# Kernel tuning notes

Measured on AMD Instinct MI355X. Metric: run time of the kernel, lower is better.

Reference implementation:

```python
import jax, jax.numpy as jnp
import numpy as np

N_NODES = 100000
N_EDGES = 1600000
D = 64            # embedding_dim
D2 = D * D        # GRUCell hidden/input size


def gru_cell(x, h, w_ih, w_hh, b_ih, b_hh):
    # PyTorch GRUCell math. x, h: [D2]; w_ih, w_hh: [3*D2, D2]; b_*: [3*D2]
    gi = w_ih @ x + b_ih
    gh = w_hh @ h + b_hh
    i_r, i_z, i_n = jnp.split(gi, 3)
    h_r, h_z, h_n = jnp.split(gh, 3)
    r = jax.nn.sigmoid(i_r + h_r)
    z = jax.nn.sigmoid(i_z + h_z)
    n = jnp.tanh(i_n + r * h_n)
    return (1.0 - z) * n + z * h


def gcn_layer(x, w, src, dst, edge_norm):
    # dense transform then degree-normalized gather-scatter aggregation
    h = x @ w                                   # [N, D]
    m = h[src] * edge_norm[:, None]             # [E, D] messages
    return jax.ops.segment_sum(m, dst, num_segments=N_NODES)


def setup_inputs() -> dict:
    key = jax.random.key(0)
    ks = jax.random.split(key, 12)
    s = 0.02  # keep GRU gates in a sane range
    return {
        "node_embeddings": jax.random.normal(ks[0], (N_NODES, D), jnp.float32),
        "gc1_weights": jax.random.normal(ks[1], (D, D), jnp.float32) * s,
        "gc2_weights": jax.random.normal(ks[2], (D, D), jnp.float32) * s,
        "gc1_hist": jax.random.normal(ks[3], (D, D), jnp.float32) * s,
        "gc2_hist": jax.random.normal(ks[4], (D, D), jnp.float32) * s,
        "w_ih": jax.random.normal(ks[5], (3 * D2, D2), jnp.float32) * s,
        "w_hh": jax.random.normal(ks[6], (3 * D2, D2), jnp.float32) * s,
        "b_ih": jax.random.normal(ks[7], (3 * D2,), jnp.float32) * s,
        "b_hh": jax.random.normal(ks[8], (3 * D2,), jnp.float32) * s,
        "src": jax.random.randint(ks[9], (N_EDGES,), 0, N_NODES, jnp.int32),
        "dst": jax.random.randint(ks[10], (N_EDGES,), 0, N_NODES, jnp.int32),
    }


def reference(node_embeddings, gc1_weights, gc2_weights, gc1_hist, gc2_hist,
              w_ih, w_hh, b_ih, b_hh, src, dst):
    # --- weight evolution (GRUCell over flattened GCN weights) ---
    w1 = gru_cell(gc1_hist.reshape(-1), gc1_weights.reshape(-1),
                  w_ih, w_hh, b_ih, b_hh).reshape(D, D)
    w2 = gru_cell(gc2_hist.reshape(-1), gc2_weights.reshape(-1),
                  w_ih, w_hh, b_ih, b_hh).reshape(D, D)

    # --- symmetric degree normalization (in-degree, clamped at 1) ---
    deg = jax.ops.segment_sum(jnp.ones_like(dst, jnp.float32), dst,
                              num_segments=N_NODES)
    norm = jnp.clip(deg, 1.0, None) ** -0.5     # [N]
    edge_norm = norm[src] * norm[dst]           # [E]

    # --- two GCN layers ---
    x = jax.nn.relu(gcn_layer(node_embeddings, w1, src, dst, edge_norm))
    x = gcn_layer(x, w2, src, dst, edge_norm)
    return x
```

## Files before the change

### kernel.cpp

```cpp
#include <hip/hip_runtime.h>

typedef unsigned int uint_t;
typedef float v4f __attribute__((ext_vector_type(4)));

#define N_NODES 100000
#define N_EDGES 1600000
#define D 64
#define D2 4096
#define D3 12288

#define NPAD 100352u

#define BSHIFT 9
#define BNODES 512
#define NBUCK 196
#define CHUNK 8192
#define CAP   16384
#define GRUBLK 3072
#define XBLK  ((N_NODES + 255) / 256)

#define OFF_GI1   0u
#define OFF_GI2   (OFF_GI1 + D3)
#define OFF_GH1   (OFF_GI2 + D3)
#define OFF_GH2   (OFF_GH1 + D3)
#define OFF_DEG   (OFF_GH2 + D3)
#define OFF_BCUR  (OFF_DEG + NPAD)
#define OFF_ROWS  (OFF_BCUR + 256u)
#define OFF_CSR   (OFF_ROWS + NPAD)
#define OFF_H     (OFF_CSR + 1600000u)
#define OFF_AGG1  (OFF_H + 3200000u)
#define OFF_PAIRS (OFF_AGG1 + 3200000u)

__device__ __forceinline__ float dot4v(v4f a, float4 b, float acc) {
    acc = fmaf(a[0], b.x, acc);
    acc = fmaf(a[1], b.y, acc);
    acc = fmaf(a[2], b.z, acc);
    acc = fmaf(a[3], b.w, acc);
    return acc;
}

__device__ __forceinline__ uint_t bfr(float f) {
    uint_t u = __float_as_uint(f);
    u += 0x7FFFu + ((u >> 16) & 1u);
    return u >> 16;
}

struct PartLds {
    int hist[256];
    int lbase[256];
    int gbase[256];
    int lcur[256];
    int2 stage[CHUNK];
};
struct GruLds {
    float4 sA[1024];
    float4 sB[1024];
};

__global__ __launch_bounds__(512) void mega1(
    const float* __restrict__ w_ih, const float* __restrict__ w_hh,
    const float* __restrict__ x1, const float* __restrict__ x2,
    const float* __restrict__ h1, const float* __restrict__ h2,
    float* __restrict__ gi1, float* __restrict__ gi2,
    float* __restrict__ gh1, float* __restrict__ gh2,
    const int* __restrict__ src, const int* __restrict__ dst,
    int* __restrict__ deg, int* __restrict__ bcur, int2* __restrict__ pairs)
{
    __shared__ __align__(16) char ldsraw[sizeof(PartLds)];
    const int tid = threadIdx.x;

    if (blockIdx.x < NBUCK) {
        PartLds& P = *reinterpret_cast<PartLds*>(ldsraw);
        const int e0  = blockIdx.x * CHUNK;
        const int cnt = min(CHUNK, N_EDGES - e0);

        if (tid < 256) { P.hist[tid] = 0; P.lcur[tid] = 0; }
        __syncthreads();
        for (int i = tid; i < cnt; i += 512) {
            const int d = dst[e0 + i];
            atomicAdd(&deg[d], 1);
            atomicAdd(&P.hist[d >> BSHIFT], 1);
        }
        __syncthreads();
        if (tid < 256) P.lbase[tid] = P.hist[tid];
        __syncthreads();
        for (int off = 1; off < 256; off <<= 1) {
            int a = 0, b = 0;
            if (tid < 256) { a = P.lbase[tid]; b = (tid >= off) ? P.lbase[tid - off] : 0; }
            __syncthreads();
            if (tid < 256) P.lbase[tid] = a + b;
            __syncthreads();
        }
        if (tid < 256) {
            const int c = P.hist[tid];
            P.lbase[tid] -= c;
            P.gbase[tid] = c ? atomicAdd(&bcur[tid], c) : 0;
        }
        __syncthreads();
        for (int i = tid; i < cnt; i += 512) {
            const int s = src[e0 + i], d = dst[e0 + i];
            const int b = d >> BSHIFT;
            const int p = P.lbase[b] + atomicAdd(&P.lcur[b], 1);
            P.stage[p] = make_int2(s, d);
        }
        __syncthreads();
        for (int i = tid; i < cnt; i += 512) {
            const int2 v = P.stage[i];
            const int b = v.y >> BSHIFT;
            const int gp = P.gbase[b] + (i - P.lbase[b]);
            if (gp < CAP) pairs[(size_t)b * CAP + gp] = v;
        }
    } else {
        GruLds& G = *reinterpret_cast<GruLds*>(ldsraw);
        const int gb   = blockIdx.x - NBUCK;
        const int half = (gb >= GRUBLK / 2);
        const int blk  = gb - (half ? GRUBLK / 2 : 0);

        {
            const float4* va = (const float4*)(half ? h1 : x1);
            const float4* vb = (const float4*)(half ? h2 : x2);
#pragma unroll
            for (int i = 0; i < 2; ++i) {
                const int k = tid + i * 512;
                G.sA[k] = va[k];
                G.sB[k] = vb[k];
            }
        }
        __syncthreads();

        const int wave = tid >> 6, lane = tid & 63;
        const int row  = blk * 8 + wave;
        const v4f* wr = (const v4f*)((half ? w_hh : w_ih) + (size_t)row * D2);

        float p0 = 0.f, p1 = 0.f;
#pragma unroll
        for (int g = 0; g < 4; ++g) {
            v4f a[4];
#pragma unroll
            for (int k = 0; k < 4; ++k)
                a[k] = __builtin_nontemporal_load(&wr[lane + (g * 4 + k) * 64]);
#pragma unroll
            for (int k = 0; k < 4; ++k) {
                const int idx = lane + (g * 4 + k) * 64;
                p0 = dot4v(a[k], G.sA[idx], p0);
                p1 = dot4v(a[k], G.sB[idx], p1);
            }
        }
#pragma unroll
        for (int m = 32; m > 0; m >>= 1) {
            p0 += __shfl_down(p0, m, 64);
            p1 += __shfl_down(p1, m, 64);
        }
        if (lane == 0) {
            float* oA = half ? gh1 : gi1;
            float* oB = half ? gh2 : gi2;
            oA[row] = p0;
            oB[row] = p1;
        }
    }
}

struct CsrLds {
    int lofs[BNODES];
    int lcur[BNODES];
    int pscan[256];
    int bscan[256];
    int stage[CAP];
};

__global__ __launch_bounds__(256) void mega2(
    const int2* __restrict__ pairs, const int* __restrict__ deg,
    const int* __restrict__ bcnt, int* __restrict__ rowstart,
    int* __restrict__ csr_src,
    const float* __restrict__ emb,
    const float* __restrict__ gi, const float* __restrict__ gh,
    const float* __restrict__ b_ih, const float* __restrict__ b_hh,
    const float* __restrict__ hw, unsigned short* __restrict__ outbf)
{
    __shared__ __align__(16) char ldsraw[sizeof(CsrLds)];
    const int tid = threadIdx.x;

    if (blockIdx.x < NBUCK) {
        CsrLds& L = *reinterpret_cast<CsrLds*>(ldsraw);
        const int b = blockIdx.x;
        const int nodeBase = b << BSHIFT;

        const int cb = (tid < NBUCK) ? bcnt[tid] : 0;
        L.bscan[tid] = cb;
        __syncthreads();
        for (int off = 1; off < 256; off <<= 1) {
            int a = L.bscan[tid];
            int x = (tid >= off) ? L.bscan[tid - off] : 0;
            __syncthreads();
            L.bscan[tid] = a + x;
            __syncthreads();
        }
        const int cnt  = bcnt[b];
        const int base = L.bscan[b] - cnt;

        const int n0 = nodeBase + 2 * tid;
        const int d0 = (n0     < N_NODES) ? deg[n0]     : 0;
        const int d1 = (n0 + 1 < N_NODES) ? deg[n0 + 1] : 0;
        L.pscan[tid] = d0 + d1;
        __syncthreads();
        for (int off = 1; off < 256; off <<= 1) {
            int a = L.pscan[tid];
            int x = (tid >= off) ? L.pscan[tid - off] : 0;
            __syncthreads();
            L.pscan[tid] = a + x;
            __syncthreads();
        }
        const int ex = L.pscan[tid] - (d0 + d1);
        L.lofs[2 * tid]     = ex;
        L.lofs[2 * tid + 1] = ex + d0;
        L.lcur[2 * tid]     = 0;
        L.lcur[2 * tid + 1] = 0;

        if (n0     < N_NODES) rowstart[n0]     = base + ex;
        if (n0 + 1 < N_NODES) rowstart[n0 + 1] = base + ex + d0;
        __syncthreads();

        const int2* bp = pairs + (size_t)b * CAP;
        for (int i = tid; i < cnt; i += 256) {
            const int2 v = bp[i];
            const int ln = v.y - nodeBase;
            const int p  = L.lofs[ln] + atomicAdd(&L.lcur[ln], 1);
            L.stage[p] = v.x;
        }
        __syncthreads();
        for (int i = tid; i < cnt; i += 256)
            csr_src[base + i] = L.stage[i];
    } else {
        float* sw = reinterpret_cast<float*>(ldsraw);
#pragma unroll
        for (int i = 0; i < 16; ++i) {
            const int j = tid + i * 256;
            float ir = gi[j]          + b_ih[j];
            float hr = gh[j]          + b_hh[j];
            float iz = gi[j + D2]     + b_ih[j + D2];
            float hz = gh[j + D2]     + b_hh[j + D2];
            float in_ = gi[j + 2*D2]  + b_ih[j + 2*D2];
            float hn = gh[j + 2*D2]   + b_hh[j + 2*D2];
            float r = 1.f / (1.f + expf(-(ir + hr)));
            float z = 1.f / (1.f + expf(-(iz + hz)));
            float n = tanhf(in_ + r * hn);
            sw[j] = (1.f - z) * n + z * hw[j];
        }
        __syncthreads();

        const int node = (blockIdx.x - NBUCK) * 256 + tid;
        if (node >= N_NODES) return;

        float x[D];
        const float4* p = (const float4*)(emb + (size_t)node * D);
#pragma unroll
        for (int i = 0; i < 16; ++i) {
            float4 u = p[i];
            x[i*4+0] = u.x; x[i*4+1] = u.y;
            x[i*4+2] = u.z; x[i*4+3] = u.w;
        }

        float acc[D];
#pragma unroll
        for (int j = 0; j < D; ++j) acc[j] = 0.f;
#pragma unroll
        for (int k = 0; k < D; ++k) {
            float a = x[k];
#pragma unroll
            for (int j = 0; j < D; ++j) acc[j] = fmaf(a, sw[k * D + j], acc[j]);
        }

        const float nn = rsqrtf(fmaxf((float)deg[node], 1.0f));
        uint_t pk[32];
#pragma unroll
        for (int j = 0; j < 32; ++j)
            pk[j] = bfr(acc[2 * j] * nn) | (bfr(acc[2 * j + 1] * nn) << 16);

        uint4* po = (uint4*)(outbf + (size_t)node * D);
#pragma unroll
        for (int i = 0; i < 8; ++i)
            po[i] = make_uint4(pk[4*i], pk[4*i+1], pk[4*i+2], pk[4*i+3]);
    }
}

__global__ __launch_bounds__(256) void transform2_kernel(
    const unsigned short* __restrict__ xin,
    const float* __restrict__ gi, const float* __restrict__ gh,
    const float* __restrict__ b_ih, const float* __restrict__ b_hh,
    const float* __restrict__ hw,
    const int* __restrict__ deg, unsigned short* __restrict__ outbf)
{
    __shared__ float sw[D * D];
    const int tid = threadIdx.x;
#pragma unroll
    for (int i = 0; i < 16; ++i) {
        const int j = tid + i * 256;
        float ir = gi[j]          + b_ih[j];
        float hr = gh[j]          + b_hh[j];
        float iz = gi[j + D2]     + b_ih[j + D2];
        float hz = gh[j + D2]     + b_hh[j + D2];
        float in_ = gi[j + 2*D2]  + b_ih[j + 2*D2];
        float hn = gh[j + 2*D2]   + b_hh[j + 2*D2];
        float r = 1.f / (1.f + expf(-(ir + hr)));
        float z = 1.f / (1.f + expf(-(iz + hz)));
        float n = tanhf(in_ + r * hn);
        sw[j] = (1.f - z) * n + z * hw[j];
    }
    __syncthreads();

    const int node = blockIdx.x * 256 + tid;
    if (node >= N_NODES) return;

    float x[D];
    const uint4* p = (const uint4*)(xin + (size_t)node * D);
#pragma unroll
    for (int i = 0; i < 8; ++i) {
        uint4 u = p[i];
        x[i*8+0] = __uint_as_float(u.x << 16);
        x[i*8+1] = __uint_as_float(u.x & 0xFFFF0000u);
        x[i*8+2] = __uint_as_float(u.y << 16);
        x[i*8+3] = __uint_as_float(u.y & 0xFFFF0000u);
        x[i*8+4] = __uint_as_float(u.z << 16);
        x[i*8+5] = __uint_as_float(u.z & 0xFFFF0000u);
        x[i*8+6] = __uint_as_float(u.w << 16);
        x[i*8+7] = __uint_as_float(u.w & 0xFFFF0000u);
    }

    float acc[D];
#pragma unroll
    for (int j = 0; j < D; ++j) acc[j] = 0.f;
#pragma unroll
    for (int k = 0; k < D; ++k) {
        float a = x[k];
#pragma unroll
        for (int j = 0; j < D; ++j) acc[j] = fmaf(a, sw[k * D + j], acc[j]);
    }

    const float nn = rsqrtf(fmaxf((float)deg[node], 1.0f));
    uint_t pk[32];
#pragma unroll
    for (int j = 0; j < 32; ++j)
        pk[j] = bfr(acc[2 * j] * nn) | (bfr(acc[2 * j + 1] * nn) << 16);

    uint4* po = (uint4*)(outbf + (size_t)node * D);
#pragma unroll
    for (int i = 0; i < 8; ++i)
        po[i] = make_uint4(pk[4*i], pk[4*i+1], pk[4*i+2], pk[4*i+3]);
}

template <bool BF16RELU_OUT>
__global__ __launch_bounds__(256) void aggregate_gather(
    const unsigned short* __restrict__ hbf, const int* __restrict__ csr_src,
    const int* __restrict__ rowstart, const int* __restrict__ degv,
    void* __restrict__ out)
{
    const int tid  = threadIdx.x;
    const int node = blockIdx.x * 32 + (tid >> 3);
    if (node >= N_NODES) return;
    const int lg = tid & 7;
    const uint4* hp = (const uint4*)hbf;

    const int beg = rowstart[node];
    const int dg  = degv[node];

    float acc[8];
#pragma unroll
    for (int c = 0; c < 8; ++c) acc[c] = 0.f;

    int k = 0;
    for (; k + 8 <= dg; k += 8) {
        int s[8];
#pragma unroll
        for (int u = 0; u < 8; ++u) s[u] = csr_src[beg + k + u];
        uint4 r[8];
#pragma unroll
        for (int u = 0; u < 8; ++u) r[u] = hp[(size_t)s[u] * 8 + lg];
#pragma unroll
        for (int u = 0; u < 8; ++u) {
            acc[0] += __uint_as_float(r[u].x << 16);
            acc[1] += __uint_as_float(r[u].x & 0xFFFF0000u);
            acc[2] += __uint_as_float(r[u].y << 16);
            acc[3] += __uint_as_float(r[u].y & 0xFFFF0000u);
            acc[4] += __uint_as_float(r[u].z << 16);
            acc[5] += __uint_as_float(r[u].z & 0xFFFF0000u);
            acc[6] += __uint_as_float(r[u].w << 16);
            acc[7] += __uint_as_float(r[u].w & 0xFFFF0000u);
        }
    }
    for (; k < dg; ++k) {
        const int s = csr_src[beg + k];
        const uint4 r = hp[(size_t)s * 8 + lg];
        acc[0] += __uint_as_float(r.x << 16);
        acc[1] += __uint_as_float(r.x & 0xFFFF0000u);
        acc[2] += __uint_as_float(r.y << 16);
        acc[3] += __uint_as_float(r.y & 0xFFFF0000u);
        acc[4] += __uint_as_float(r.z << 16);
        acc[5] += __uint_as_float(r.z & 0xFFFF0000u);
        acc[6] += __uint_as_float(r.w << 16);
        acc[7] += __uint_as_float(r.w & 0xFFFF0000u);
    }

    const float nn = rsqrtf(fmaxf((float)dg, 1.0f));
    if (BF16RELU_OUT) {
        float o[8];
#pragma unroll
        for (int c = 0; c < 8; ++c) o[c] = fmaxf(acc[c] * nn, 0.f);
        uint4 pk;
        pk.x = bfr(o[0]) | (bfr(o[1]) << 16);
        pk.y = bfr(o[2]) | (bfr(o[3]) << 16);
        pk.z = bfr(o[4]) | (bfr(o[5]) << 16);
        pk.w = bfr(o[6]) | (bfr(o[7]) << 16);
        ((uint4*)out)[(size_t)node * 8 + lg] = pk;
    } else {
        float* op = (float*)out + (size_t)node * D + (size_t)lg * 8;
        *(float4*)(op)     = make_float4(acc[0]*nn, acc[1]*nn, acc[2]*nn, acc[3]*nn);
        *(float4*)(op + 4) = make_float4(acc[4]*nn, acc[5]*nn, acc[6]*nn, acc[7]*nn);
    }
}

extern "C" void kernel_launch(void* const* d_in, const int* in_sizes, int n_in,
                              void* d_out, int out_size, void* d_ws, size_t ws_size,
                              hipStream_t stream)
{
    const float* emb  = (const float*)d_in[0];
    const float* gc1w = (const float*)d_in[1];
    const float* gc2w = (const float*)d_in[2];
    const float* gc1h = (const float*)d_in[3];
    const float* gc2h = (const float*)d_in[4];
    const float* w_ih = (const float*)d_in[5];
    const float* w_hh = (const float*)d_in[6];
    const float* b_ih = (const float*)d_in[7];
    const float* b_hh = (const float*)d_in[8];
    const int* src = (const int*)d_in[9];
    const int* dst = (const int*)d_in[10];

    float* ws = (float*)d_ws;
    float* gi1 = ws + OFF_GI1;
    float* gi2 = ws + OFF_GI2;
    float* gh1 = ws + OFF_GH1;
    float* gh2 = ws + OFF_GH2;
    int*   deg = (int*)(ws + OFF_DEG);
    int*   bcur = (int*)(ws + OFF_BCUR);
    int*   rows = (int*)(ws + OFF_ROWS);
    int*   csr  = (int*)(ws + OFF_CSR);
    unsigned short* hbf  = (unsigned short*)(ws + OFF_H);
    unsigned short* agg1 = (unsigned short*)(ws + OFF_AGG1);
    int2*  pairs = (int2*)(ws + OFF_PAIRS);
    float* out  = (float*)d_out;

    hipMemsetAsync(deg, 0, (NPAD + 256) * sizeof(int), stream);

    mega1<<<NBUCK + GRUBLK, 512, 0, stream>>>(
        w_ih, w_hh, gc1h, gc2h, gc1w, gc2w, gi1, gi2, gh1, gh2,
        src, dst, deg, bcur, pairs);

    mega2<<<NBUCK + XBLK, 256, 0, stream>>>(
        pairs, deg, bcur, rows, csr,
        emb, gi1, gh1, b_ih, b_hh, gc1w, hbf);

    aggregate_gather<true><<<(N_NODES + 31) / 32, 256, 0, stream>>>(
        hbf, csr, rows, deg, agg1);

    transform2_kernel<<<XBLK, 256, 0, stream>>>(
        agg1, gi2, gh2, b_ih, b_hh, gc2w, deg, hbf);
    aggregate_gather<false><<<(N_NODES + 31) / 32, 256, 0, stream>>>(
        hbf, csr, rows, deg, out);
}
```

Baseline: 619.9 us.

## Reorder GCN as aggregate-then-transform and fuse matmul into gather kernel

Uses linearity, (A·X)·W = A·(X·W), to gather source rows first and then apply the 64x64 weight in the same kernel, with the aggregated row staged in LDS. The evolved GRU weights are computed once by two dedicated blocks and written to workspace, and the per-node transform kernels go away. The first pass now only scales the embeddings by norm and converts them to bf16. This removes one full-size intermediate write and read plus a launch. In exchange, each 256-thread block reloads the 16 KB weight into LDS and adds a block barrier, and ReLU and the norm are now applied after the matmul in a different order.

```diff
diff --git a/kernel.cpp b/kernel.cpp
--- a/kernel.cpp
+++ b/kernel.cpp
@@ -23,13 +23,15 @@
 #define OFF_GI2   (OFF_GI1 + D3)
 #define OFF_GH1   (OFF_GI2 + D3)
 #define OFF_GH2   (OFF_GH1 + D3)
-#define OFF_DEG   (OFF_GH2 + D3)
+#define OFF_W1    (OFF_GH2 + D3)
+#define OFF_W2    (OFF_W1 + D2)
+#define OFF_DEG   (OFF_W2 + D2)
 #define OFF_BCUR  (OFF_DEG + NPAD)
 #define OFF_ROWS  (OFF_BCUR + 256u)
 #define OFF_CSR   (OFF_ROWS + NPAD)
-#define OFF_H     (OFF_CSR + 1600000u)
-#define OFF_AGG1  (OFF_H + 3200000u)
-#define OFF_PAIRS (OFF_AGG1 + 3200000u)
+#define OFF_XP    (OFF_CSR + 1600000u)
+#define OFF_Y1    (OFF_XP + 3200000u)
+#define OFF_PAIRS (OFF_Y1 + 3200000u)
 
 __device__ __forceinline__ float dot4v(v4f a, float4 b, float acc) {
     acc = fmaf(a[0], b.x, acc);
@@ -173,9 +175,12 @@
     const int* __restrict__ bcnt, int* __restrict__ rowstart,
     int* __restrict__ csr_src,
     const float* __restrict__ emb,
-    const float* __restrict__ gi, const float* __restrict__ gh,
+    const float* __restrict__ gi1, const float* __restrict__ gh1,
+    const float* __restrict__ gi2, const float* __restrict__ gh2,
     const float* __restrict__ b_ih, const float* __restrict__ b_hh,
-    const float* __restrict__ hw, unsigned short* __restrict__ outbf)
+    const float* __restrict__ hw1, const float* __restrict__ hw2,
+    float* __restrict__ w1, float* __restrict__ w2,
+    unsigned short* __restrict__ xp)
 {
     __shared__ __align__(16) char ldsraw[sizeof(CsrLds)];
     const int tid = threadIdx.x;
@@ -230,8 +235,12 @@
         __syncthreads();
         for (int i = tid; i < cnt; i += 256)
             csr_src[base + i] = L.stage[i];
-    } else {
-        float* sw = reinterpret_cast<float*>(ldsraw);
+    } else if (blockIdx.x < NBUCK + 2) {
+        const int layer = blockIdx.x - NBUCK;
+        const float* gi = layer ? gi2 : gi1;
+        const float* gh = layer ? gh2 : gh1;
+        const float* hw = layer ? hw2 : hw1;
+        float* wo = layer ? w2 : w1;
 #pragma unroll
         for (int i = 0; i < 16; ++i) {
             const int j = tid + i * 256;
@@ -244,177 +253,122 @@
             float r = 1.f / (1.f + expf(-(ir + hr)));
             float z = 1.f / (1.f + expf(-(iz + hz)));
             float n = tanhf(in_ + r * hn);
-            sw[j] = (1.f - z) * n + z * hw[j];
-        }
-        __syncthreads();
-
-        const int node = (blockIdx.x - NBUCK) * 256 + tid;
+            wo[j] = (1.f - z) * n + z * hw[j];
+        }
+    } else {
+        const int node = (blockIdx.x - NBUCK - 2) * 256 + tid;
         if (node >= N_NODES) return;
-
-        float x[D];
+        const float nn = rsqrtf(fmaxf((float)deg[node], 1.0f));
         const float4* p = (const float4*)(emb + (size_t)node * D);
+        uint_t pk[32];
 #pragma unroll
         for (int i = 0; i < 16; ++i) {
             float4 u = p[i];
-            x[i*4+0] = u.x; x[i*4+1] = u.y;
-            x[i*4+2] = u.z; x[i*4+3] = u.w;
-        }
-
-        float acc[D];
-#pragma unroll
-        for (int j = 0; j < D; ++j) acc[j] = 0.f;
-#pragma unroll
-        for (int k = 0; k < D; ++k) {
-            float a = x[k];
-#pragma unroll
-            for (int j = 0; j < D; ++j) acc[j] = fmaf(a, sw[k * D + j], acc[j]);
-        }
-
-        const float nn = rsqrtf(fmaxf((float)deg[node], 1.0f));
-        uint_t pk[32];
-#pragma unroll
-        for (int j = 0; j < 32; ++j)
-            pk[j] = bfr(acc[2 * j] * nn) | (bfr(acc[2 * j + 1] * nn) << 16);
-
-        uint4* po = (uint4*)(outbf + (size_t)node * D);
+            pk[2*i]   = bfr(u.x * nn) | (bfr(u.y * nn) << 16);
+            pk[2*i+1] = bfr(u.z * nn) | (bfr(u.w * nn) << 16);
+        }
+        uint4* po = (uint4*)(xp + (size_t)node * D);
 #pragma unroll
         for (int i = 0; i < 8; ++i)
             po[i] = make_uint4(pk[4*i], pk[4*i+1], pk[4*i+2], pk[4*i+3]);
     }
 }
 
-__global__ __launch_bounds__(256) void transform2_kernel(
-    const unsigned short* __restrict__ xin,
-    const float* __restrict__ gi, const float* __restrict__ gh,
-    const float* __restrict__ b_ih, const float* __restrict__ b_hh,
-    const float* __restrict__ hw,
-    const int* __restrict__ deg, unsigned short* __restrict__ outbf)
+template <bool LAYER1>
+__global__ __launch_bounds__(256) void gcn_layer_kernel(
+    const unsigned short* __restrict__ xbf, const float* __restrict__ w,
+    const int* __restrict__ csr_src, const int* __restrict__ rowstart,
+    const int* __restrict__ degv, void* __restrict__ out)
 {
-    __shared__ float sw[D * D];
+    __shared__ float sw[D2];
+    __shared__ float xr[4][8][68];
     const int tid = threadIdx.x;
 #pragma unroll
-    for (int i = 0; i < 16; ++i) {
-        const int j = tid + i * 256;
-        float ir = gi[j]          + b_ih[j];
-        float hr = gh[j]          + b_hh[j];
-        float iz = gi[j + D2]     + b_ih[j + D2];
-        float hz = gh[j + D2]     + b_hh[j + D2];
-        float in_ = gi[j + 2*D2]  + b_ih[j + 2*D2];
-        float hn = gh[j + 2*D2]   + b_hh[j + 2*D2];
-        float r = 1.f / (1.f + expf(-(ir + hr)));
-        float z = 1.f / (1.f + expf(-(iz + hz)));
-        float n = tanhf(in_ + r * hn);
-        sw[j] = (1.f - z) * n + z * hw[j];
+    for (int i = 0; i < 16; ++i) sw[tid + i * 256] = w[tid + i * 256];
+    __syncthreads();
+
+    const int node = blockIdx.x * 32 + (tid >> 3);
+    const int lg   = tid & 7;
+    const int wv   = tid >> 6;
+    const int slot = (tid >> 3) & 7;
+    const uint4* hp = (const uint4*)xbf;
+    const bool active = (node < N_NODES);
+    int dg = 0;
+
+    if (active) {
+        const int beg = rowstart[node];
+        dg = degv[node];
+
+        float acc[8];
+#pragma unroll
+        for (int c = 0; c < 8; ++c) acc[c] = 0.f;
+
+        int k = 0;
+        for (; k + 8 <= dg; k += 8) {
+            int s[8];
+#pragma unroll
+            for (int u = 0; u < 8; ++u) s[u] = csr_src[beg + k + u];
+            uint4 r[8];
+#pragma unroll
+            for (int u = 0; u < 8; ++u) r[u] = hp[(size_t)s[u] * 8 + lg];
+#pragma unroll
+            for (int u = 0; u < 8; ++u) {
+                acc[0] += __uint_as_float(r[u].x << 16);
+                acc[1] += __uint_as_float(r[u].x & 0xFFFF0000u);
+                acc[2] += __uint_as_float(r[u].y << 16);
+                acc[3] += __uint_as_float(r[u].y & 0xFFFF0000u);
+                acc[4] += __uint_as_float(r[u].z << 16);
+                acc[5] += __uint_as_float(r[u].z & 0xFFFF0000u);
+                acc[6] += __uint_as_float(r[u].w << 16);
+                acc[7] += __uint_as_float(r[u].w & 0xFFFF0000u);
+            }
+        }
+        for (; k < dg; ++k) {
+            const int s = csr_src[beg + k];
+            const uint4 r = hp[(size_t)s * 8 + lg];
+            acc[0] += __uint_as_float(r.x << 16);
+            acc[1] += __uint_as_float(r.x & 0xFFFF0000u);
+            acc[2] += __uint_as_float(r.y << 16);
+            acc[3] += __uint_as_float(r.y & 0xFFFF0000u);
+            acc[4] += __uint_as_float(r.z << 16);
+            acc[5] += __uint_as_float(r.z & 0xFFFF0000u);
+            acc[6] += __uint_as_float(r.w << 16);
+            acc[7] += __uint_as_float(r.w & 0xFFFF0000u);
+        }
+
+        const float nn = rsqrtf(fmaxf((float)dg, 1.0f));
+#pragma unroll
+        for (int c = 0; c < 8; ++c) xr[wv][slot][lg * 8 + c] = acc[c] * nn;
     }
     __syncthreads();
 
-    const int node = blockIdx.x * 256 + tid;
-    if (node >= N_NODES) return;
-
-    float x[D];
-    const uint4* p = (const uint4*)(xin + (size_t)node * D);
-#pragma unroll
-    for (int i = 0; i < 8; ++i) {
-        uint4 u = p[i];
-        x[i*8+0] = __uint_as_float(u.x << 16);
-        x[i*8+1] = __uint_as_float(u.x & 0xFFFF0000u);
-        x[i*8+2] = __uint_as_float(u.y << 16);
-        x[i*8+3] = __uint_as_float(u.y & 0xFFFF0000u);
-        x[i*8+4] = __uint_as_float(u.z << 16);
-        x[i*8+5] = __uint_as_float(u.z & 0xFFFF0000u);
-        x[i*8+6] = __uint_as_float(u.w << 16);
-        x[i*8+7] = __uint_as_float(u.w & 0xFFFF0000u);
-    }
-
-    float acc[D];
-#pragma unroll
-    for (int j = 0; j < D; ++j) acc[j] = 0.f;
-#pragma unroll
-    for (int k = 0; k < D; ++k) {
-        float a = x[k];
-#pragma unroll
-        for (int j = 0; j < D; ++j) acc[j] = fmaf(a, sw[k * D + j], acc[j]);
-    }
-
-    const float nn = rsqrtf(fmaxf((float)deg[node], 1.0f));
-    uint_t pk[32];
-#pragma unroll
-    for (int j = 0; j < 32; ++j)
-        pk[j] = bfr(acc[2 * j] * nn) | (bfr(acc[2 * j + 1] * nn) << 16);
-
-    uint4* po = (uint4*)(outbf + (size_t)node * D);
-#pragma unroll
-    for (int i = 0; i < 8; ++i)
-        po[i] = make_uint4(pk[4*i], pk[4*i+1], pk[4*i+2], pk[4*i+3]);
-}
-
-template <bool BF16RELU_OUT>
-__global__ __launch_bounds__(256) void aggregate_gather(
-    const unsigned short* __restrict__ hbf, const int* __restrict__ csr_src,
-    const int* __restrict__ rowstart, const int* __restrict__ degv,
-    void* __restrict__ out)
-{
-    const int tid  = threadIdx.x;
-    const int node = blockIdx.x * 32 + (tid >> 3);
-    if (node >= N_NODES) return;
-    const int lg = tid & 7;
-    const uint4* hp = (const uint4*)hbf;
-
-    const int beg = rowstart[node];
-    const int dg  = degv[node];
-
-    float acc[8];
-#pragma unroll
-    for (int c = 0; c < 8; ++c) acc[c] = 0.f;
-
-    int k = 0;
-    for (; k + 8 <= dg; k += 8) {
-        int s[8];
-#pragma unroll
-        for (int u = 0; u < 8; ++u) s[u] = csr_src[beg + k + u];
-        uint4 r[8];
-#pragma unroll
-        for (int u = 0; u < 8; ++u) r[u] = hp[(size_t)s[u] * 8 + lg];
-#pragma unroll
-        for (int u = 0; u < 8; ++u) {
-            acc[0] += __uint_as_float(r[u].x << 16);
-            acc[1] += __uint_as_float(r[u].x & 0xFFFF0000u);
-            acc[2] += __uint_as_float(r[u].y << 16);
-            acc[3] += __uint_as_float(r[u].y & 0xFFFF0000u);
-            acc[4] += __uint_as_float(r[u].z << 16);
-            acc[5] += __uint_as_float(r[u].z & 0xFFFF0000u);
-            acc[6] += __uint_as_float(r[u].w << 16);
-            acc[7] += __uint_as_float(r[u].w & 0xFFFF0000u);
-        }
-    }
-    for (; k < dg; ++k) {
-        const int s = csr_src[beg + k];
-        const uint4 r = hp[(size_t)s * 8 + lg];
-        acc[0] += __uint_as_float(r.x << 16);
-        acc[1] += __uint_as_float(r.x & 0xFFFF0000u);
-        acc[2] += __uint_as_float(r.y << 16);
-        acc[3] += __uint_as_float(r.y & 0xFFFF0000u);
-        acc[4] += __uint_as_float(r.z << 16);
-        acc[5] += __uint_as_float(r.z & 0xFFFF0000u);
-        acc[6] += __uint_as_float(r.w << 16);
-        acc[7] += __uint_as_float(r.w & 0xFFFF0000u);
-    }
-
-    const float nn = rsqrtf(fmaxf((float)dg, 1.0f));
-    if (BF16RELU_OUT) {
+    if (active) {
         float o[8];
 #pragma unroll
-        for (int c = 0; c < 8; ++c) o[c] = fmaxf(acc[c] * nn, 0.f);
-        uint4 pk;
-        pk.x = bfr(o[0]) | (bfr(o[1]) << 16);
-        pk.y = bfr(o[2]) | (bfr(o[3]) << 16);
-        pk.z = bfr(o[4]) | (bfr(o[5]) << 16);
-        pk.w = bfr(o[6]) | (bfr(o[7]) << 16);
-        ((uint4*)out)[(size_t)node * 8 + lg] = pk;
-    } else {
-        float* op = (float*)out + (size_t)node * D + (size_t)lg * 8;
-        *(float4*)(op)     = make_float4(acc[0]*nn, acc[1]*nn, acc[2]*nn, acc[3]*nn);
-        *(float4*)(op + 4) = make_float4(acc[4]*nn, acc[5]*nn, acc[6]*nn, acc[7]*nn);
+        for (int c = 0; c < 8; ++c) o[c] = 0.f;
+#pragma unroll
+        for (int k = 0; k < D; ++k) {
+            const float xv = xr[wv][slot][k];
+#pragma unroll
+            for (int c = 0; c < 8; ++c)
+                o[c] = fmaf(xv, sw[k * D + lg * 8 + c], o[c]);
+        }
+        if (LAYER1) {
+            const float nn = rsqrtf(fmaxf((float)dg, 1.0f));
+            float t[8];
+#pragma unroll
+            for (int c = 0; c < 8; ++c) t[c] = fmaxf(o[c], 0.f) * nn;
+            uint4 pk;
+            pk.x = bfr(t[0]) | (bfr(t[1]) << 16);
+            pk.y = bfr(t[2]) | (bfr(t[3]) << 16);
+            pk.z = bfr(t[4]) | (bfr(t[5]) << 16);
+            pk.w = bfr(t[6]) | (bfr(t[7]) << 16);
+            ((uint4*)out)[(size_t)node * 8 + lg] = pk;
+        } else {
+            float* op = (float*)out + (size_t)node * D + (size_t)lg * 8;
+            *(float4*)(op)     = make_float4(o[0], o[1], o[2], o[3]);
+            *(float4*)(op + 4) = make_float4(o[4], o[5], o[6], o[7]);
+        }
     }
 }
 
@@ -439,12 +393,14 @@
     float* gi2 = ws + OFF_GI2;
     float* gh1 = ws + OFF_GH1;
     float* gh2 = ws + OFF_GH2;
+    float* w1  = ws + OFF_W1;
+    float* w2  = ws + OFF_W2;
     int*   deg = (int*)(ws + OFF_DEG);
     int*   bcur = (int*)(ws + OFF_BCUR);
     int*   rows = (int*)(ws + OFF_ROWS);
     int*   csr  = (int*)(ws + OFF_CSR);
-    unsigned short* hbf  = (unsigned short*)(ws + OFF_H);
-    unsigned short* agg1 = (unsigned short*)(ws + OFF_AGG1);
+    unsigned short* xp = (unsigned short*)(ws + OFF_XP);
+    unsigned short* y1 = (unsigned short*)(ws + OFF_Y1);
     int2*  pairs = (int2*)(ws + OFF_PAIRS);
     float* out  = (float*)d_out;
 
@@ -454,15 +410,13 @@
         w_ih, w_hh, gc1h, gc2h, gc1w, gc2w, gi1, gi2, gh1, gh2,
         src, dst, deg, bcur, pairs);
 
-    mega2<<<NBUCK + XBLK, 256, 0, stream>>>(
-        pairs, deg, bcur, rows, csr,
-        emb, gi1, gh1, b_ih, b_hh, gc1w, hbf);
-
-    aggregate_gather<true><<<(N_NODES + 31) / 32, 256, 0, stream>>>(
-        hbf, csr, rows, deg, agg1);
-
-    transform2_kernel<<<XBLK, 256, 0, stream>>>(
-        agg1, gi2, gh2, b_ih, b_hh, gc2w, deg, hbf);
-    aggregate_gather<false><<<(N_NODES + 31) / 32, 256, 0, stream>>>(
-        hbf, csr, rows, deg, out);
-}
+    mega2<<<NBUCK + 2 + XBLK, 256, 0, stream>>>(
+        pairs, deg, bcur, rows, csr, emb,
+        gi1, gh1, gi2, gh2, b_ih, b_hh, gc1w, gc2w, w1, w2, xp);
+
+    gcn_layer_kernel<true><<<(N_NODES + 31) / 32, 256, 0, stream>>>(
+        xp, w1, csr, rows, deg, y1);
+
+    gcn_layer_kernel<false><<<(N_NODES + 31) / 32, 256, 0, stream>>>(
+        y1, w2, csr, rows, deg, out);
+}
```

After: 569.5 us, median of 2. -8.1%, faster.
